# Kernel optimization log

Measured on AMD Instinct MI355X. Metric: run time of the kernel, lower is better.

The kernel has to match this reference:

```python
import jax, jax.numpy as jnp
import numpy as np

N_NODES = 20000
N_EDGES = 160000
IN_DIM = 512
HID = 256
N_CLASSES = 2
NUM_GRAPHS = 16


def setup_inputs() -> dict:
    key = jax.random.key(0)
    ks = jax.random.split(key, 12)
    x = jax.random.normal(ks[0], (N_NODES, IN_DIM), dtype=jnp.float32)
    edge_index = jax.random.randint(ks[1], (2, N_EDGES), 0, N_NODES, dtype=jnp.int64)
    batch = jnp.sort(jax.random.randint(ks[2], (N_NODES,), 0, NUM_GRAPHS, dtype=jnp.int64))
    def glorot(k, shape):
        lim = float(np.sqrt(6.0 / (shape[0] + shape[1])))
        return jax.random.uniform(k, shape, jnp.float32, -lim, lim)
    return {
        "x": x,
        "edge_index": edge_index,
        "batch": batch,
        "W1n": glorot(ks[3], (IN_DIM, HID)),
        "W1s": glorot(ks[4], (IN_DIM, HID)),
        "b1": jnp.zeros((HID,), jnp.float32),
        "W2n": glorot(ks[5], (HID, HID)),
        "W2s": glorot(ks[6], (HID, HID)),
        "b2": jnp.zeros((HID,), jnp.float32),
        "fc1w": glorot(ks[7], (HID, HID // 2)),
        "fc1b": jnp.zeros((HID // 2,), jnp.float32),
        "fc2w": glorot(ks[8], (HID // 2, N_CLASSES)),
        "fc2b": jnp.zeros((N_CLASSES,), jnp.float32),
    }


def _sage_conv(x, W_nbr, W_self, b, src, dst, n_nodes):
    # mean-aggregate neighbor features (messages flow src -> dst, PyG convention)
    deg = jax.ops.segment_sum(jnp.ones(src.shape, x.dtype), dst, num_segments=n_nodes)
    deg = jnp.maximum(deg, 1.0)
    aggr = jax.ops.segment_sum(x[src], dst, num_segments=n_nodes) / deg[:, None]
    # SAGEConv: lin_l(aggr) + lin_r(x) + bias (equivalent to concat-linear)
    return aggr @ W_nbr + x @ W_self + b


def reference(x, edge_index, batch, W1n, W1s, b1, W2n, W2s, b2, fc1w, fc1b, fc2w, fc2b):
    src, dst = edge_index[0], edge_index[1]
    n = x.shape[0]
    h = jax.nn.relu(_sage_conv(x, W1n, W1s, b1, src, dst, n))
    h = jax.nn.relu(_sage_conv(h, W2n, W2s, b2, src, dst, n))
    # global_mean_pool over graph ids
    cnt = jax.ops.segment_sum(jnp.ones((n,), h.dtype), batch, num_segments=NUM_GRAPHS)
    pooled = jax.ops.segment_sum(h, batch, num_segments=NUM_GRAPHS) / jnp.maximum(cnt, 1.0)[:, None]
    out = jax.nn.relu(pooled @ fc1w + fc1b) @ fc2w + fc2b
    return out
```

## Files before the change

### kernel.cpp

```cpp
#include <hip/hip_runtime.h>
#include <hip/hip_bf16.h>


#define HID 256
#define NCOL 512

typedef __bf16 bf16x8 __attribute__((ext_vector_type(8)));
typedef float floatx4 __attribute__((ext_vector_type(4)));
typedef ushort ushort8v __attribute__((ext_vector_type(8)));
typedef unsigned int u32;
typedef const u32 __attribute__((address_space(1)))* gp_t;
typedef u32 __attribute__((address_space(3)))* lp_t;

__device__ __forceinline__ ushort f2bf(float f) {
    unsigned u = __float_as_uint(f);
    u += 0x7fffu + ((u >> 16) & 1u);
    return (ushort)(u >> 16);
}
__device__ __forceinline__ float bf2f(ushort b) {
    return __uint_as_float(((unsigned)b) << 16);
}

__device__ __forceinline__ void packT_work(const float* __restrict__ Wn,
                                           const float* __restrict__ Ws,
                                           ushort* __restrict__ WT, int K, int gid) {
    if (gid >= NCOL * K) return;
    int n = gid / K, k = gid - n * K;
    float v = (n < HID) ? Wn[k * HID + n] : Ws[k * HID + (n - HID)];
    WT[gid] = f2bf(v);
}

__global__ void prep_kernel(const float* __restrict__ x, ushort* __restrict__ xb, int n4,
                            const float* __restrict__ W1n, const float* __restrict__ W1s,
                            ushort* __restrict__ w1t, int K1,
                            const float* __restrict__ W2n, const float* __restrict__ W2s,
                            ushort* __restrict__ w2t, int K2,
                            const int* __restrict__ dst, int* __restrict__ degi, int n_edges,
                            int nb_cvt, int nb_w1, int nb_w2) {
    int bx = blockIdx.x, t = threadIdx.x;
    if (bx < nb_cvt) {
        int i = bx * 256 + t;
        if (i < n4) {
            float4 v = ((const float4*)x)[i];
            ushort4 o;
            o.x = f2bf(v.x); o.y = f2bf(v.y); o.z = f2bf(v.z); o.w = f2bf(v.w);
            ((ushort4*)xb)[i] = o;
        }
    } else if (bx < nb_cvt + nb_w1) {
        packT_work(W1n, W1s, w1t, K1, (bx - nb_cvt) * 256 + t);
    } else if (bx < nb_cvt + nb_w1 + nb_w2) {
        packT_work(W2n, W2s, w2t, K2, (bx - nb_cvt - nb_w1) * 256 + t);
    } else {
        int e = (bx - nb_cvt - nb_w1 - nb_w2) * 256 + t;
        if (e < n_edges) atomicAdd(&degi[dst[e]], 1);
    }
}

__global__ __launch_bounds__(256) void psum_kernel(const int* __restrict__ degi,
                                                   int* __restrict__ partials, int n) {
    int t = threadIdx.x;
    int i = blockIdx.x * 256 + t;
    int v = (i < n) ? degi[i] : 0;
#pragma unroll
    for (int d = 1; d < 64; d <<= 1) v += __shfl_xor(v, d, 64);
    __shared__ int wsum[4];
    if ((t & 63) == 0) wsum[t >> 6] = v;
    __syncthreads();
    if (t == 0) partials[blockIdx.x] = wsum[0] + wsum[1] + wsum[2] + wsum[3];
}

__global__ __launch_bounds__(256) void scan2_kernel(const int* __restrict__ degi,
                                                    const int* __restrict__ partials,
                                                    int* __restrict__ off,
                                                    int* __restrict__ cursor, int n, int nb) {
    int t = threadIdx.x, lane = t & 63, w = t >> 6;
    int c = blockIdx.x;
    int pre = 0, tot = 0;
    for (int base = 0; base < nb; base += 64) {
        int idx = base + lane;
        int pv = (idx < nb) ? partials[idx] : 0;
        pre += (idx < c) ? pv : 0;
        tot += pv;
    }
#pragma unroll
    for (int d = 1; d < 64; d <<= 1) {
        pre += __shfl_xor(pre, d, 64);
        tot += __shfl_xor(tot, d, 64);
    }
    if (c == 0 && t == 0) off[n] = tot;
    int i = c * 256 + t;
    int v = (i < n) ? degi[i] : 0;
    int s = v;
#pragma unroll
    for (int d = 1; d < 64; d <<= 1) {
        int u = __shfl_up(s, d, 64);
        if (lane >= d) s += u;
    }
    __shared__ int wsum[4];
    if (lane == 63) wsum[w] = s;
    __syncthreads();
    int woff = 0;
    for (int k = 0; k < w; ++k) woff += wsum[k];
    int excl = pre + woff + s - v;
    if (i < n) { off[i] = excl; cursor[i] = excl; }
}

__global__ void fill_kernel(const int* __restrict__ src, const int* __restrict__ dst,
                            int* __restrict__ cursor, int* __restrict__ eidx, int n_edges) {
    int e = blockIdx.x * 256 + threadIdx.x;
    if (e < n_edges) {
        int p = atomicAdd(&cursor[dst[e]], 1);
        eidx[p] = src[e];
    }
}

__global__ __launch_bounds__(256) void gemm_mfma(const ushort* __restrict__ A,
                                                 const ushort* __restrict__ BT,
                                                 ushort* __restrict__ Yn,
                                                 ushort* __restrict__ Ys, int K, int nG) {
    int b = blockIdx.x;
    int xcd = b & 7, rest = b >> 3;
    int m = rest & 3, Ggrp = rest >> 2;
    int G = xcd + 8 * Ggrp;
    if (G >= nG) return;
    int m0 = G * 64, n0 = m * 128;

    __shared__ ushort As[2][64 * 64];
    __shared__ ushort Bs[2][128 * 64];
    int tid = threadIdx.x;
    int w = tid >> 6, lane = tid & 63;
    int quad = lane >> 4, r16 = lane & 15;
    int wm = (w >> 1) * 32, wn = (w & 1) * 64;

    int arow[2], agu[2], brow[4], bgu[4];
#pragma unroll
    for (int rr = 0; rr < 2; ++rr) {
        int idx = rr * 256 + tid;
        arow[rr] = idx >> 3;
        agu[rr] = (idx & 7) ^ (arow[rr] & 7);
    }
#pragma unroll
    for (int rr = 0; rr < 4; ++rr) {
        int idx = rr * 256 + tid;
        brow[rr] = idx >> 3;
        bgu[rr] = (idx & 7) ^ (brow[rr] & 7);
    }

    auto stage = [&](int buf, int k0) {
#pragma unroll
        for (int rr = 0; rr < 2; ++rr) {
            const ushort* ga = A + (size_t)(m0 + arow[rr]) * K + k0 + agu[rr] * 8;
            ushort* la = As[buf] + (size_t)(rr * 256 + w * 64) * 8;
            __builtin_amdgcn_global_load_lds((gp_t)(const void*)ga, (lp_t)(void*)la, 16, 0, 0);
        }
#pragma unroll
        for (int rr = 0; rr < 4; ++rr) {
            const ushort* gb = BT + (size_t)(n0 + brow[rr]) * K + k0 + bgu[rr] * 8;
            ushort* lb = Bs[buf] + (size_t)(rr * 256 + w * 64) * 8;
            __builtin_amdgcn_global_load_lds((gp_t)(const void*)gb, (lp_t)(void*)lb, 16, 0, 0);
        }
    };

    floatx4 acc[2][4];
#pragma unroll
    for (int i = 0; i < 2; ++i)
#pragma unroll
        for (int j = 0; j < 4; ++j) acc[i][j] = (floatx4){0.f, 0.f, 0.f, 0.f};

    const int nk = K >> 6;
    stage(0, 0);
    for (int t = 0; t < nk; ++t) {
        int cb = t & 1;
        __syncthreads();
        if (t + 1 < nk) stage(cb ^ 1, (t + 1) << 6);
        const ushort* Ab = As[cb];
        const ushort* Bb = Bs[cb];
#pragma unroll
        for (int s = 0; s < 2; ++s) {
            bf16x8 a[2], b2[4];
#pragma unroll
            for (int i = 0; i < 2; ++i) {
                int row = wm + i * 16 + r16;
                int au = (s * 4 + quad) ^ (row & 7);
                a[i] = *(const bf16x8*)(Ab + row * 64 + au * 8);
            }
#pragma unroll
            for (int j = 0; j < 4; ++j) {
                int row = wn + j * 16 + r16;
                int bu = (s * 4 + quad) ^ (row & 7);
                b2[j] = *(const bf16x8*)(Bb + row * 64 + bu * 8);
            }
#pragma unroll
            for (int i = 0; i < 2; ++i)
#pragma unroll
                for (int j = 0; j < 4; ++j)
                    acc[i][j] = __builtin_amdgcn_mfma_f32_16x16x32_bf16(a[i], b2[j], acc[i][j], 0, 0, 0);
        }
    }
    ushort* O = (m < 2) ? Yn : Ys;
    int cb0 = (m < 2) ? n0 : (n0 - 256);
#pragma unroll
    for (int i = 0; i < 2; ++i)
#pragma unroll
        for (int j = 0; j < 4; ++j) {
            int col = cb0 + wn + j * 16 + r16;
#pragma unroll
            for (int rg = 0; rg < 4; ++rg) {
                int row = m0 + wm + i * 16 + quad * 4 + rg;
                O[(size_t)row * HID + col] = f2bf(acc[i][j][rg]);
            }
        }
}

__device__ __forceinline__ void acc8(float* A, ushort8v y) {
#pragma unroll
    for (int i = 0; i < 8; ++i) A[i] += bf2f((ushort)y[i]);
}

__global__ __launch_bounds__(256) void gather_kernel(const ushort* __restrict__ Yn,
                                                     const ushort* __restrict__ Ys,
                                                     const int* __restrict__ off,
                                                     const int* __restrict__ eidx,
                                                     const float* __restrict__ bias,
                                                     ushort* __restrict__ h, int n_nodes) {
    int tid = threadIdx.x;
    int v = blockIdx.x * 4 + (tid >> 6);
    if (v >= n_nodes) return;
    int lane = tid & 63;
    int half = lane >> 5, sub = lane & 31;
    int c8 = sub << 3;
    int e0 = off[v], e1 = off[v + 1];
    float accA[8] = {0.f, 0.f, 0.f, 0.f, 0.f, 0.f, 0.f, 0.f};
    float accB[8] = {0.f, 0.f, 0.f, 0.f, 0.f, 0.f, 0.f, 0.f};
    for (int base = e0; base < e1; base += 64) {
        int ecnt = min(64, e1 - base);
        int ev = (lane < ecnt) ? eidx[base + lane] : 0;
        int j = 0;
        for (; j + 16 <= ecnt; j += 16) {
            int s0 = __shfl(ev, j + 0 + half, 64);
            int s1 = __shfl(ev, j + 2 + half, 64);
            int s2 = __shfl(ev, j + 4 + half, 64);
            int s3 = __shfl(ev, j + 6 + half, 64);
            int s4 = __shfl(ev, j + 8 + half, 64);
            int s5 = __shfl(ev, j + 10 + half, 64);
            int s6 = __shfl(ev, j + 12 + half, 64);
            int s7 = __shfl(ev, j + 14 + half, 64);
            ushort8v y0 = *(const ushort8v*)(Yn + (size_t)s0 * HID + c8);
            ushort8v y1 = *(const ushort8v*)(Yn + (size_t)s1 * HID + c8);
            ushort8v y2 = *(const ushort8v*)(Yn + (size_t)s2 * HID + c8);
            ushort8v y3 = *(const ushort8v*)(Yn + (size_t)s3 * HID + c8);
            ushort8v y4 = *(const ushort8v*)(Yn + (size_t)s4 * HID + c8);
            ushort8v y5 = *(const ushort8v*)(Yn + (size_t)s5 * HID + c8);
            ushort8v y6 = *(const ushort8v*)(Yn + (size_t)s6 * HID + c8);
            ushort8v y7 = *(const ushort8v*)(Yn + (size_t)s7 * HID + c8);
            acc8(accA, y0); acc8(accB, y1); acc8(accA, y2); acc8(accB, y3);
            acc8(accA, y4); acc8(accB, y5); acc8(accA, y6); acc8(accB, y7);
        }
        for (; j < ecnt; j += 2) {
            int idx = j + half;
            if (idx < ecnt) {
                int s = __shfl(ev, idx, 64);
                ushort8v y = *(const ushort8v*)(Yn + (size_t)s * HID + c8);
                acc8(accA, y);
            }
        }
    }
#pragma unroll
    for (int i = 0; i < 8; ++i) {
        accA[i] += accB[i];
        accA[i] += __shfl_xor(accA[i], 32, 64);
    }
    if (half == 0) {
        ushort8v sv = *(const ushort8v*)(Ys + (size_t)v * HID + c8);
        float bb[8];
        *(float4*)(bb)     = *(const float4*)(bias + c8);
        *(float4*)(bb + 4) = *(const float4*)(bias + c8 + 4);
        float invd = 1.0f / fmaxf((float)(e1 - e0), 1.0f);
        ushort8v r;
#pragma unroll
        for (int i = 0; i < 8; ++i)
            r[i] = f2bf(fmaxf(accA[i] * invd + bf2f((ushort)sv[i]) + bb[i], 0.f));
        *(ushort8v*)(h + (size_t)v * HID + c8) = r;
    }
}

__global__ void pool_kernel(const ushort* __restrict__ h, const int* __restrict__ batch,
                            float* __restrict__ pooled, float* __restrict__ cnt, int n_nodes) {
    int f = threadIdx.x;
    int v0 = blockIdx.x * 64;
    int vend = min(v0 + 64, n_nodes);
    if (v0 >= n_nodes) return;
    int cur = batch[v0];
    float acc = 0.f, ac = 0.f;
    for (int v = v0; v < vend; ++v) {
        int g = batch[v];
        if (g != cur) {
            atomicAdd(&pooled[cur * HID + f], acc);
            if (f == 0) atomicAdd(&cnt[cur], ac);
            acc = 0.f; ac = 0.f; cur = g;
        }
        acc += bf2f(h[(size_t)v * HID + f]);
        ac += 1.0f;
    }
    atomicAdd(&pooled[cur * HID + f], acc);
    if (f == 0) atomicAdd(&cnt[cur], ac);
}

__global__ void head_kernel(const float* __restrict__ pooled, const float* __restrict__ cnt,
                            const float* __restrict__ fc1w, const float* __restrict__ fc1b,
                            const float* __restrict__ fc2w, const float* __restrict__ fc2b,
                            float* __restrict__ out) {
    int g = blockIdx.x, j = threadIdx.x;
    __shared__ float p[256];
    __shared__ float hid[128];
    float inv = 1.0f / fmaxf(cnt[g], 1.0f);
    p[j] = pooled[g * HID + j] * inv;
    p[j + 128] = pooled[g * HID + 128 + j] * inv;
    __syncthreads();
    float a = fc1b[j];
    for (int f = 0; f < 256; ++f) a += p[f] * fc1w[f * 128 + j];
    hid[j] = fmaxf(a, 0.f);
    __syncthreads();
    if (j < 2) {
        float o = fc2b[j];
        for (int t = 0; t < 128; ++t) o += hid[t] * fc2w[t * 2 + j];
        out[g * 2 + j] = o;
    }
}

extern "C" void kernel_launch(void* const* d_in, const int* in_sizes, int n_in,
                              void* d_out, int out_size, void* d_ws, size_t ws_size,
                              hipStream_t stream) {
    const float* x    = (const float*)d_in[0];
    const int*   ei   = (const int*)d_in[1];
    const int*   batch= (const int*)d_in[2];
    const float* W1n  = (const float*)d_in[3];
    const float* W1s  = (const float*)d_in[4];
    const float* b1   = (const float*)d_in[5];
    const float* W2n  = (const float*)d_in[6];
    const float* W2s  = (const float*)d_in[7];
    const float* b2   = (const float*)d_in[8];
    const float* fc1w = (const float*)d_in[9];
    const float* fc1b = (const float*)d_in[10];
    const float* fc2w = (const float*)d_in[11];
    const float* fc2b = (const float*)d_in[12];
    float* out = (float*)d_out;

    const int n_nodes = in_sizes[2];
    const int n_edges = in_sizes[1] / 2;
    const int in_dim  = in_sizes[0] / n_nodes;
    const int Mpad    = (n_nodes + 63) & ~63;
    const int nb      = (n_nodes + 255) / 256;
    const int nG      = Mpad / 64;
    const int* src = ei;
    const int* dst = ei + n_edges;

    char* wsb = (char*)d_ws;
    size_t cur = 0;
    auto alloc = [&](size_t nbytes) { size_t o = cur; cur = (cur + nbytes + 255) & ~(size_t)255; return o; };
    size_t o_degi = alloc((size_t)n_nodes * 4);
    size_t o_pool = alloc((size_t)16 * HID * 4 + 16 * 4);
    size_t zero_end = cur;
    size_t o_off  = alloc((size_t)(n_nodes + 1) * 4);
    size_t o_cur  = alloc((size_t)n_nodes * 4);
    size_t o_part = alloc((size_t)nb * 4);
    size_t o_eidx = alloc((size_t)n_edges * 4);
    size_t o_w1   = alloc((size_t)NCOL * in_dim * 2);
    size_t o_w2   = alloc((size_t)NCOL * HID * 2);
    size_t o_xb   = alloc((size_t)Mpad * in_dim * 2);
    size_t o_hb   = alloc((size_t)Mpad * HID * 2);
    size_t o_yn   = alloc((size_t)Mpad * HID * 2);
    size_t o_ys   = alloc((size_t)Mpad * HID * 2);
    (void)ws_size;

    int*    degi    = (int*)(wsb + o_degi);
    float*  pooled  = (float*)(wsb + o_pool);
    float*  cnt     = pooled + 16 * HID;
    int*    off     = (int*)(wsb + o_off);
    int*    cursor  = (int*)(wsb + o_cur);
    int*    partials= (int*)(wsb + o_part);
    int*    eidx    = (int*)(wsb + o_eidx);
    ushort* w1t     = (ushort*)(wsb + o_w1);
    ushort* w2t     = (ushort*)(wsb + o_w2);
    ushort* xb      = (ushort*)(wsb + o_xb);
    ushort* hb      = (ushort*)(wsb + o_hb);
    ushort* Yn      = (ushort*)(wsb + o_yn);
    ushort* Ys      = (ushort*)(wsb + o_ys);

    hipMemsetAsync(wsb + o_degi, 0, zero_end - o_degi, stream);

    int n4 = n_nodes * in_dim / 4;
    int nb_cvt = (n4 + 255) / 256;
    int nb_w1  = (NCOL * in_dim + 255) / 256;
    int nb_w2  = (NCOL * HID + 255) / 256;
    int nb_deg = (n_edges + 255) / 256;
    prep_kernel<<<nb_cvt + nb_w1 + nb_w2 + nb_deg, 256, 0, stream>>>(
        x, xb, n4, W1n, W1s, w1t, in_dim, W2n, W2s, w2t, HID,
        dst, degi, n_edges, nb_cvt, nb_w1, nb_w2);

    psum_kernel<<<nb, 256, 0, stream>>>(degi, partials, n_nodes);
    scan2_kernel<<<nb, 256, 0, stream>>>(degi, partials, off, cursor, n_nodes, nb);
    fill_kernel<<<(n_edges + 255) / 256, 256, 0, stream>>>(src, dst, cursor, eidx, n_edges);

    int gemm_blocks = 8 * 4 * ((nG + 7) / 8);
    int gather_blocks = (n_nodes + 3) / 4;

    gemm_mfma<<<gemm_blocks, 256, 0, stream>>>(xb, w1t, Yn, Ys, in_dim, nG);
    gather_kernel<<<gather_blocks, 256, 0, stream>>>(Yn, Ys, off, eidx, b1, hb, n_nodes);

    gemm_mfma<<<gemm_blocks, 256, 0, stream>>>(hb, w2t, Yn, Ys, HID, nG);
    gather_kernel<<<gather_blocks, 256, 0, stream>>>(Yn, Ys, off, eidx, b2, hb, n_nodes);

    pool_kernel<<<(n_nodes + 63) / 64, 256, 0, stream>>>(hb, batch, pooled, cnt, n_nodes);
    head_kernel<<<16, 128, 0, stream>>>(pooled, cnt, fc1w, fc1b, fc2w, fc2b, out);
}
```

Measured before the change: 223.7 us.

## Fuse all stages into one persistent kernel with atomic grid barriers

Replaces the sequence of ten kernel launches (prep, scan, fill, two GEMMs, two gathers, pool, head) with a single persistent kernel of 512 blocks that loops over work with grid-stride loops and separates phases with atomic-counter grid barriers. The fill of the CSR edge index now overlaps with the first GEMM in the same phase. This removes per-launch overhead and inter-kernel idle gaps. In exchange, the GEMM and gather lose the XCD-aware tile ordering and the full-grid parallelism, and the barrier spin relies on all 512 blocks being co-resident.

```diff
diff --git a/kernel.cpp b/kernel.cpp
--- a/kernel.cpp
+++ b/kernel.cpp
@@ -4,6 +4,8 @@
 
 #define HID 256
 #define NCOL 512
+#define NB 512
+#define NTHR 256
 
 typedef __bf16 bf16x8 __attribute__((ext_vector_type(8)));
 typedef float floatx4 __attribute__((ext_vector_type(4)));
@@ -21,112 +23,30 @@
     return __uint_as_float(((unsigned)b) << 16);
 }
 
+__device__ __forceinline__ void gsync(u32* bar, int slot) {
+    __syncthreads();
+    if (threadIdx.x == 0) {
+        __threadfence();
+        __hip_atomic_fetch_add(bar + slot, 1u, __ATOMIC_RELEASE, __HIP_MEMORY_SCOPE_AGENT);
+        while (__hip_atomic_load(bar + slot, __ATOMIC_ACQUIRE, __HIP_MEMORY_SCOPE_AGENT) < NB)
+            __builtin_amdgcn_s_sleep(8);
+        __threadfence();
+    }
+    __syncthreads();
+}
+
 __device__ __forceinline__ void packT_work(const float* __restrict__ Wn,
                                            const float* __restrict__ Ws,
                                            ushort* __restrict__ WT, int K, int gid) {
-    if (gid >= NCOL * K) return;
     int n = gid / K, k = gid - n * K;
     float v = (n < HID) ? Wn[k * HID + n] : Ws[k * HID + (n - HID)];
     WT[gid] = f2bf(v);
 }
 
-__global__ void prep_kernel(const float* __restrict__ x, ushort* __restrict__ xb, int n4,
-                            const float* __restrict__ W1n, const float* __restrict__ W1s,
-                            ushort* __restrict__ w1t, int K1,
-                            const float* __restrict__ W2n, const float* __restrict__ W2s,
-                            ushort* __restrict__ w2t, int K2,
-                            const int* __restrict__ dst, int* __restrict__ degi, int n_edges,
-                            int nb_cvt, int nb_w1, int nb_w2) {
-    int bx = blockIdx.x, t = threadIdx.x;
-    if (bx < nb_cvt) {
-        int i = bx * 256 + t;
-        if (i < n4) {
-            float4 v = ((const float4*)x)[i];
-            ushort4 o;
-            o.x = f2bf(v.x); o.y = f2bf(v.y); o.z = f2bf(v.z); o.w = f2bf(v.w);
-            ((ushort4*)xb)[i] = o;
-        }
-    } else if (bx < nb_cvt + nb_w1) {
-        packT_work(W1n, W1s, w1t, K1, (bx - nb_cvt) * 256 + t);
-    } else if (bx < nb_cvt + nb_w1 + nb_w2) {
-        packT_work(W2n, W2s, w2t, K2, (bx - nb_cvt - nb_w1) * 256 + t);
-    } else {
-        int e = (bx - nb_cvt - nb_w1 - nb_w2) * 256 + t;
-        if (e < n_edges) atomicAdd(&degi[dst[e]], 1);
-    }
-}
-
-__global__ __launch_bounds__(256) void psum_kernel(const int* __restrict__ degi,
-                                                   int* __restrict__ partials, int n) {
-    int t = threadIdx.x;
-    int i = blockIdx.x * 256 + t;
-    int v = (i < n) ? degi[i] : 0;
-#pragma unroll
-    for (int d = 1; d < 64; d <<= 1) v += __shfl_xor(v, d, 64);
-    __shared__ int wsum[4];
-    if ((t & 63) == 0) wsum[t >> 6] = v;
-    __syncthreads();
-    if (t == 0) partials[blockIdx.x] = wsum[0] + wsum[1] + wsum[2] + wsum[3];
-}
-
-__global__ __launch_bounds__(256) void scan2_kernel(const int* __restrict__ degi,
-                                                    const int* __restrict__ partials,
-                                                    int* __restrict__ off,
-                                                    int* __restrict__ cursor, int n, int nb) {
-    int t = threadIdx.x, lane = t & 63, w = t >> 6;
-    int c = blockIdx.x;
-    int pre = 0, tot = 0;
-    for (int base = 0; base < nb; base += 64) {
-        int idx = base + lane;
-        int pv = (idx < nb) ? partials[idx] : 0;
-        pre += (idx < c) ? pv : 0;
-        tot += pv;
-    }
-#pragma unroll
-    for (int d = 1; d < 64; d <<= 1) {
-        pre += __shfl_xor(pre, d, 64);
-        tot += __shfl_xor(tot, d, 64);
-    }
-    if (c == 0 && t == 0) off[n] = tot;
-    int i = c * 256 + t;
-    int v = (i < n) ? degi[i] : 0;
-    int s = v;
-#pragma unroll
-    for (int d = 1; d < 64; d <<= 1) {
-        int u = __shfl_up(s, d, 64);
-        if (lane >= d) s += u;
-    }
-    __shared__ int wsum[4];
-    if (lane == 63) wsum[w] = s;
-    __syncthreads();
-    int woff = 0;
-    for (int k = 0; k < w; ++k) woff += wsum[k];
-    int excl = pre + woff + s - v;
-    if (i < n) { off[i] = excl; cursor[i] = excl; }
-}
-
-__global__ void fill_kernel(const int* __restrict__ src, const int* __restrict__ dst,
-                            int* __restrict__ cursor, int* __restrict__ eidx, int n_edges) {
-    int e = blockIdx.x * 256 + threadIdx.x;
-    if (e < n_edges) {
-        int p = atomicAdd(&cursor[dst[e]], 1);
-        eidx[p] = src[e];
-    }
-}
-
-__global__ __launch_bounds__(256) void gemm_mfma(const ushort* __restrict__ A,
-                                                 const ushort* __restrict__ BT,
-                                                 ushort* __restrict__ Yn,
-                                                 ushort* __restrict__ Ys, int K, int nG) {
-    int b = blockIdx.x;
-    int xcd = b & 7, rest = b >> 3;
-    int m = rest & 3, Ggrp = rest >> 2;
-    int G = xcd + 8 * Ggrp;
-    if (G >= nG) return;
-    int m0 = G * 64, n0 = m * 128;
-
-    __shared__ ushort As[2][64 * 64];
-    __shared__ ushort Bs[2][128 * 64];
+__device__ __forceinline__ void gemm_tiles(const ushort* __restrict__ A,
+                                           const ushort* __restrict__ BT,
+                                           ushort* __restrict__ Yn, ushort* __restrict__ Ys,
+                                           int K, int nG, ushort* As0, ushort* Bs0) {
     int tid = threadIdx.x;
     int w = tid >> 6, lane = tid & 63;
     int quad = lane >> 4, r16 = lane & 15;
@@ -146,70 +66,77 @@
         bgu[rr] = (idx & 7) ^ (brow[rr] & 7);
     }
 
-    auto stage = [&](int buf, int k0) {
-#pragma unroll
-        for (int rr = 0; rr < 2; ++rr) {
-            const ushort* ga = A + (size_t)(m0 + arow[rr]) * K + k0 + agu[rr] * 8;
-            ushort* la = As[buf] + (size_t)(rr * 256 + w * 64) * 8;
-            __builtin_amdgcn_global_load_lds((gp_t)(const void*)ga, (lp_t)(void*)la, 16, 0, 0);
-        }
-#pragma unroll
-        for (int rr = 0; rr < 4; ++rr) {
-            const ushort* gb = BT + (size_t)(n0 + brow[rr]) * K + k0 + bgu[rr] * 8;
-            ushort* lb = Bs[buf] + (size_t)(rr * 256 + w * 64) * 8;
-            __builtin_amdgcn_global_load_lds((gp_t)(const void*)gb, (lp_t)(void*)lb, 16, 0, 0);
-        }
-    };
-
-    floatx4 acc[2][4];
-#pragma unroll
-    for (int i = 0; i < 2; ++i)
-#pragma unroll
-        for (int j = 0; j < 4; ++j) acc[i][j] = (floatx4){0.f, 0.f, 0.f, 0.f};
-
-    const int nk = K >> 6;
-    stage(0, 0);
-    for (int t = 0; t < nk; ++t) {
-        int cb = t & 1;
+    const int ntile = nG * 4;
+    for (int tl = blockIdx.x; tl < ntile; tl += NB) {
+        int G = tl >> 2, m = tl & 3;
+        int m0 = G * 64, n0 = m * 128;
+
+        auto stage = [&](int buf, int k0) {
+#pragma unroll
+            for (int rr = 0; rr < 2; ++rr) {
+                const ushort* ga = A + (size_t)(m0 + arow[rr]) * K + k0 + agu[rr] * 8;
+                ushort* la = As0 + (size_t)buf * 4096 + (size_t)(rr * 256 + w * 64) * 8;
+                __builtin_amdgcn_global_load_lds((gp_t)(const void*)ga, (lp_t)(void*)la, 16, 0, 0);
+            }
+#pragma unroll
+            for (int rr = 0; rr < 4; ++rr) {
+                const ushort* gb = BT + (size_t)(n0 + brow[rr]) * K + k0 + bgu[rr] * 8;
+                ushort* lb = Bs0 + (size_t)buf * 8192 + (size_t)(rr * 256 + w * 64) * 8;
+                __builtin_amdgcn_global_load_lds((gp_t)(const void*)gb, (lp_t)(void*)lb, 16, 0, 0);
+            }
+        };
+
+        floatx4 acc[2][4];
+#pragma unroll
+        for (int i = 0; i < 2; ++i)
+#pragma unroll
+            for (int j = 0; j < 4; ++j) acc[i][j] = (floatx4){0.f, 0.f, 0.f, 0.f};
+
         __syncthreads();
-        if (t + 1 < nk) stage(cb ^ 1, (t + 1) << 6);
-        const ushort* Ab = As[cb];
-        const ushort* Bb = Bs[cb];
-#pragma unroll
-        for (int s = 0; s < 2; ++s) {
-            bf16x8 a[2], b2[4];
-#pragma unroll
-            for (int i = 0; i < 2; ++i) {
-                int row = wm + i * 16 + r16;
-                int au = (s * 4 + quad) ^ (row & 7);
-                a[i] = *(const bf16x8*)(Ab + row * 64 + au * 8);
-            }
+        stage(0, 0);
+        const int nk = K >> 6;
+        for (int t = 0; t < nk; ++t) {
+            int cb = t & 1;
+            __syncthreads();
+            if (t + 1 < nk) stage(cb ^ 1, (t + 1) << 6);
+            const ushort* Ab = As0 + cb * 4096;
+            const ushort* Bb = Bs0 + cb * 8192;
+#pragma unroll
+            for (int s = 0; s < 2; ++s) {
+                bf16x8 a[2], b2[4];
+#pragma unroll
+                for (int i = 0; i < 2; ++i) {
+                    int row = wm + i * 16 + r16;
+                    int au = (s * 4 + quad) ^ (row & 7);
+                    a[i] = *(const bf16x8*)(Ab + row * 64 + au * 8);
+                }
+#pragma unroll
+                for (int j = 0; j < 4; ++j) {
+                    int row = wn + j * 16 + r16;
+                    int bu = (s * 4 + quad) ^ (row & 7);
+                    b2[j] = *(const bf16x8*)(Bb + row * 64 + bu * 8);
+                }
+#pragma unroll
+                for (int i = 0; i < 2; ++i)
+#pragma unroll
+                    for (int j = 0; j < 4; ++j)
+                        acc[i][j] = __builtin_amdgcn_mfma_f32_16x16x32_bf16(a[i], b2[j], acc[i][j], 0, 0, 0);
+            }
+        }
+        ushort* O = (m < 2) ? Yn : Ys;
+        int cb0 = (m < 2) ? n0 : (n0 - 256);
+#pragma unroll
+        for (int i = 0; i < 2; ++i)
 #pragma unroll
             for (int j = 0; j < 4; ++j) {
-                int row = wn + j * 16 + r16;
-                int bu = (s * 4 + quad) ^ (row & 7);
-                b2[j] = *(const bf16x8*)(Bb + row * 64 + bu * 8);
-            }
-#pragma unroll
-            for (int i = 0; i < 2; ++i)
-#pragma unroll
-                for (int j = 0; j < 4; ++j)
-                    acc[i][j] = __builtin_amdgcn_mfma_f32_16x16x32_bf16(a[i], b2[j], acc[i][j], 0, 0, 0);
-        }
-    }
-    ushort* O = (m < 2) ? Yn : Ys;
-    int cb0 = (m < 2) ? n0 : (n0 - 256);
-#pragma unroll
-    for (int i = 0; i < 2; ++i)
-#pragma unroll
-        for (int j = 0; j < 4; ++j) {
-            int col = cb0 + wn + j * 16 + r16;
-#pragma unroll
-            for (int rg = 0; rg < 4; ++rg) {
-                int row = m0 + wm + i * 16 + quad * 4 + rg;
-                O[(size_t)row * HID + col] = f2bf(acc[i][j][rg]);
-            }
-        }
+                int col = cb0 + wn + j * 16 + r16;
+#pragma unroll
+                for (int rg = 0; rg < 4; ++rg) {
+                    int row = m0 + wm + i * 16 + quad * 4 + rg;
+                    O[(size_t)row * HID + col] = f2bf(acc[i][j][rg]);
+                }
+            }
+    }
 }
 
 __device__ __forceinline__ void acc8(float* A, ushort8v y) {
@@ -217,114 +144,214 @@
     for (int i = 0; i < 8; ++i) A[i] += bf2f((ushort)y[i]);
 }
 
-__global__ __launch_bounds__(256) void gather_kernel(const ushort* __restrict__ Yn,
-                                                     const ushort* __restrict__ Ys,
-                                                     const int* __restrict__ off,
-                                                     const int* __restrict__ eidx,
-                                                     const float* __restrict__ bias,
-                                                     ushort* __restrict__ h, int n_nodes) {
+__device__ __forceinline__ void gather_nodes(const ushort* __restrict__ Yn,
+                                             const ushort* __restrict__ Ys,
+                                             const int* __restrict__ off,
+                                             const int* __restrict__ eidx,
+                                             const float* __restrict__ bias,
+                                             ushort* __restrict__ h, int n_nodes) {
     int tid = threadIdx.x;
-    int v = blockIdx.x * 4 + (tid >> 6);
-    if (v >= n_nodes) return;
     int lane = tid & 63;
     int half = lane >> 5, sub = lane & 31;
     int c8 = sub << 3;
-    int e0 = off[v], e1 = off[v + 1];
-    float accA[8] = {0.f, 0.f, 0.f, 0.f, 0.f, 0.f, 0.f, 0.f};
-    float accB[8] = {0.f, 0.f, 0.f, 0.f, 0.f, 0.f, 0.f, 0.f};
-    for (int base = e0; base < e1; base += 64) {
-        int ecnt = min(64, e1 - base);
-        int ev = (lane < ecnt) ? eidx[base + lane] : 0;
-        int j = 0;
-        for (; j + 16 <= ecnt; j += 16) {
-            int s0 = __shfl(ev, j + 0 + half, 64);
-            int s1 = __shfl(ev, j + 2 + half, 64);
-            int s2 = __shfl(ev, j + 4 + half, 64);
-            int s3 = __shfl(ev, j + 6 + half, 64);
-            int s4 = __shfl(ev, j + 8 + half, 64);
-            int s5 = __shfl(ev, j + 10 + half, 64);
-            int s6 = __shfl(ev, j + 12 + half, 64);
-            int s7 = __shfl(ev, j + 14 + half, 64);
-            ushort8v y0 = *(const ushort8v*)(Yn + (size_t)s0 * HID + c8);
-            ushort8v y1 = *(const ushort8v*)(Yn + (size_t)s1 * HID + c8);
-            ushort8v y2 = *(const ushort8v*)(Yn + (size_t)s2 * HID + c8);
-            ushort8v y3 = *(const ushort8v*)(Yn + (size_t)s3 * HID + c8);
-            ushort8v y4 = *(const ushort8v*)(Yn + (size_t)s4 * HID + c8);
-            ushort8v y5 = *(const ushort8v*)(Yn + (size_t)s5 * HID + c8);
-            ushort8v y6 = *(const ushort8v*)(Yn + (size_t)s6 * HID + c8);
-            ushort8v y7 = *(const ushort8v*)(Yn + (size_t)s7 * HID + c8);
-            acc8(accA, y0); acc8(accB, y1); acc8(accA, y2); acc8(accB, y3);
-            acc8(accA, y4); acc8(accB, y5); acc8(accA, y6); acc8(accB, y7);
-        }
-        for (; j < ecnt; j += 2) {
-            int idx = j + half;
-            if (idx < ecnt) {
-                int s = __shfl(ev, idx, 64);
-                ushort8v y = *(const ushort8v*)(Yn + (size_t)s * HID + c8);
-                acc8(accA, y);
-            }
-        }
-    }
-#pragma unroll
-    for (int i = 0; i < 8; ++i) {
-        accA[i] += accB[i];
-        accA[i] += __shfl_xor(accA[i], 32, 64);
-    }
-    if (half == 0) {
-        ushort8v sv = *(const ushort8v*)(Ys + (size_t)v * HID + c8);
-        float bb[8];
-        *(float4*)(bb)     = *(const float4*)(bias + c8);
-        *(float4*)(bb + 4) = *(const float4*)(bias + c8 + 4);
-        float invd = 1.0f / fmaxf((float)(e1 - e0), 1.0f);
-        ushort8v r;
-#pragma unroll
-        for (int i = 0; i < 8; ++i)
-            r[i] = f2bf(fmaxf(accA[i] * invd + bf2f((ushort)sv[i]) + bb[i], 0.f));
-        *(ushort8v*)(h + (size_t)v * HID + c8) = r;
-    }
-}
-
-__global__ void pool_kernel(const ushort* __restrict__ h, const int* __restrict__ batch,
-                            float* __restrict__ pooled, float* __restrict__ cnt, int n_nodes) {
-    int f = threadIdx.x;
-    int v0 = blockIdx.x * 64;
-    int vend = min(v0 + 64, n_nodes);
-    if (v0 >= n_nodes) return;
-    int cur = batch[v0];
-    float acc = 0.f, ac = 0.f;
-    for (int v = v0; v < vend; ++v) {
-        int g = batch[v];
-        if (g != cur) {
-            atomicAdd(&pooled[cur * HID + f], acc);
-            if (f == 0) atomicAdd(&cnt[cur], ac);
-            acc = 0.f; ac = 0.f; cur = g;
-        }
-        acc += bf2f(h[(size_t)v * HID + f]);
-        ac += 1.0f;
-    }
-    atomicAdd(&pooled[cur * HID + f], acc);
-    if (f == 0) atomicAdd(&cnt[cur], ac);
-}
-
-__global__ void head_kernel(const float* __restrict__ pooled, const float* __restrict__ cnt,
-                            const float* __restrict__ fc1w, const float* __restrict__ fc1b,
-                            const float* __restrict__ fc2w, const float* __restrict__ fc2b,
-                            float* __restrict__ out) {
-    int g = blockIdx.x, j = threadIdx.x;
-    __shared__ float p[256];
-    __shared__ float hid[128];
-    float inv = 1.0f / fmaxf(cnt[g], 1.0f);
-    p[j] = pooled[g * HID + j] * inv;
-    p[j + 128] = pooled[g * HID + 128 + j] * inv;
-    __syncthreads();
-    float a = fc1b[j];
-    for (int f = 0; f < 256; ++f) a += p[f] * fc1w[f * 128 + j];
-    hid[j] = fmaxf(a, 0.f);
-    __syncthreads();
-    if (j < 2) {
-        float o = fc2b[j];
-        for (int t = 0; t < 128; ++t) o += hid[t] * fc2w[t * 2 + j];
-        out[g * 2 + j] = o;
+    int w0 = (blockIdx.x << 2) + (tid >> 6);
+    for (int v = w0; v < n_nodes; v += NB * 4) {
+        int e0 = off[v], e1 = off[v + 1];
+        float accA[8] = {0.f, 0.f, 0.f, 0.f, 0.f, 0.f, 0.f, 0.f};
+        float accB[8] = {0.f, 0.f, 0.f, 0.f, 0.f, 0.f, 0.f, 0.f};
+        for (int base = e0; base < e1; base += 64) {
+            int ecnt = min(64, e1 - base);
+            int ev = (lane < ecnt) ? eidx[base + lane] : 0;
+            int j = 0;
+            for (; j + 16 <= ecnt; j += 16) {
+                int s0 = __shfl(ev, j + 0 + half, 64);
+                int s1 = __shfl(ev, j + 2 + half, 64);
+                int s2 = __shfl(ev, j + 4 + half, 64);
+                int s3 = __shfl(ev, j + 6 + half, 64);
+                int s4 = __shfl(ev, j + 8 + half, 64);
+                int s5 = __shfl(ev, j + 10 + half, 64);
+                int s6 = __shfl(ev, j + 12 + half, 64);
+                int s7 = __shfl(ev, j + 14 + half, 64);
+                ushort8v y0 = *(const ushort8v*)(Yn + (size_t)s0 * HID + c8);
+                ushort8v y1 = *(const ushort8v*)(Yn + (size_t)s1 * HID + c8);
+                ushort8v y2 = *(const ushort8v*)(Yn + (size_t)s2 * HID + c8);
+                ushort8v y3 = *(const ushort8v*)(Yn + (size_t)s3 * HID + c8);
+                ushort8v y4 = *(const ushort8v*)(Yn + (size_t)s4 * HID + c8);
+                ushort8v y5 = *(const ushort8v*)(Yn + (size_t)s5 * HID + c8);
+                ushort8v y6 = *(const ushort8v*)(Yn + (size_t)s6 * HID + c8);
+                ushort8v y7 = *(const ushort8v*)(Yn + (size_t)s7 * HID + c8);
+                acc8(accA, y0); acc8(accB, y1); acc8(accA, y2); acc8(accB, y3);
+                acc8(accA, y4); acc8(accB, y5); acc8(accA, y6); acc8(accB, y7);
+            }
+            for (; j < ecnt; j += 2) {
+                int idx = j + half;
+                if (idx < ecnt) {
+                    int s = __shfl(ev, idx, 64);
+                    ushort8v y = *(const ushort8v*)(Yn + (size_t)s * HID + c8);
+                    acc8(accA, y);
+                }
+            }
+        }
+#pragma unroll
+        for (int i = 0; i < 8; ++i) {
+            accA[i] += accB[i];
+            accA[i] += __shfl_xor(accA[i], 32, 64);
+        }
+        if (half == 0) {
+            ushort8v sv = *(const ushort8v*)(Ys + (size_t)v * HID + c8);
+            float bb[8];
+            *(float4*)(bb)     = *(const float4*)(bias + c8);
+            *(float4*)(bb + 4) = *(const float4*)(bias + c8 + 4);
+            float invd = 1.0f / fmaxf((float)(e1 - e0), 1.0f);
+            ushort8v r;
+#pragma unroll
+            for (int i = 0; i < 8; ++i)
+                r[i] = f2bf(fmaxf(accA[i] * invd + bf2f((ushort)sv[i]) + bb[i], 0.f));
+            *(ushort8v*)(h + (size_t)v * HID + c8) = r;
+        }
+    }
+}
+
+__global__ __launch_bounds__(NTHR, 2) void mega(
+    const float* __restrict__ x, const int* __restrict__ src, const int* __restrict__ dst,
+    const int* __restrict__ batch,
+    const float* __restrict__ W1n, const float* __restrict__ W1s, const float* __restrict__ b1,
+    const float* __restrict__ W2n, const float* __restrict__ W2s, const float* __restrict__ b2,
+    const float* __restrict__ fc1w, const float* __restrict__ fc1b,
+    const float* __restrict__ fc2w, const float* __restrict__ fc2b,
+    float* __restrict__ out,
+    int* __restrict__ degi, float* __restrict__ pooled, float* __restrict__ cnt,
+    int* __restrict__ off, int* __restrict__ cursor, int* __restrict__ partials,
+    int* __restrict__ eidx, ushort* __restrict__ w1t, ushort* __restrict__ w2t,
+    ushort* __restrict__ xb, ushort* __restrict__ hb,
+    ushort* __restrict__ Yn, ushort* __restrict__ Ys,
+    u32* __restrict__ bar,
+    int n_nodes, int n_edges, int in_dim, int nG, int nbc, int n4) {
+
+    __shared__ ushort As[2 * 64 * 64];
+    __shared__ ushort Bs[2 * 128 * 64];
+    __shared__ int wsum[4];
+
+    const int tid = threadIdx.x, bid = blockIdx.x;
+    const int gthr = bid * NTHR + tid;
+    const int GT = NB * NTHR;
+
+    for (int i = gthr; i < n4; i += GT) {
+        float4 v = ((const float4*)x)[i];
+        ushort4 o;
+        o.x = f2bf(v.x); o.y = f2bf(v.y); o.z = f2bf(v.z); o.w = f2bf(v.w);
+        ((ushort4*)xb)[i] = o;
+    }
+    for (int g = gthr; g < NCOL * in_dim; g += GT) packT_work(W1n, W1s, w1t, in_dim, g);
+    for (int g = gthr; g < NCOL * HID; g += GT) packT_work(W2n, W2s, w2t, HID, g);
+    for (int e = gthr; e < n_edges; e += GT) atomicAdd(&degi[dst[e]], 1);
+    gsync(bar, 0);
+
+    for (int c = bid; c < nbc; c += NB) {
+        int i = c * 256 + tid;
+        int v = (i < n_nodes) ? degi[i] : 0;
+#pragma unroll
+        for (int d = 1; d < 64; d <<= 1) v += __shfl_xor(v, d, 64);
+        if ((tid & 63) == 0) wsum[tid >> 6] = v;
+        __syncthreads();
+        if (tid == 0) partials[c] = wsum[0] + wsum[1] + wsum[2] + wsum[3];
+        __syncthreads();
+    }
+    gsync(bar, 1);
+
+    {
+        int lane = tid & 63, w = tid >> 6;
+        for (int c = bid; c < nbc; c += NB) {
+            int pre = 0, tot = 0;
+            for (int base = 0; base < nbc; base += 64) {
+                int idx = base + lane;
+                int pv = (idx < nbc) ? partials[idx] : 0;
+                pre += (idx < c) ? pv : 0;
+                tot += pv;
+            }
+#pragma unroll
+            for (int d = 1; d < 64; d <<= 1) {
+                pre += __shfl_xor(pre, d, 64);
+                tot += __shfl_xor(tot, d, 64);
+            }
+            if (c == 0 && tid == 0) off[n_nodes] = tot;
+            int i = c * 256 + tid;
+            int v = (i < n_nodes) ? degi[i] : 0;
+            int s = v;
+#pragma unroll
+            for (int d = 1; d < 64; d <<= 1) {
+                int u = __shfl_up(s, d, 64);
+                if (lane >= d) s += u;
+            }
+            if (lane == 63) wsum[w] = s;
+            __syncthreads();
+            int woff = 0;
+            for (int k = 0; k < w; ++k) woff += wsum[k];
+            int excl = pre + woff + s - v;
+            if (i < n_nodes) { off[i] = excl; cursor[i] = excl; }
+            __syncthreads();
+        }
+    }
+    gsync(bar, 2);
+
+    for (int e = gthr; e < n_edges; e += GT) {
+        int p = atomicAdd(&cursor[dst[e]], 1);
+        eidx[p] = src[e];
+    }
+    gemm_tiles(xb, w1t, Yn, Ys, in_dim, nG, As, Bs);
+    gsync(bar, 3);
+
+    gather_nodes(Yn, Ys, off, eidx, b1, hb, n_nodes);
+    gsync(bar, 4);
+
+    gemm_tiles(hb, w2t, Yn, Ys, HID, nG, As, Bs);
+    gsync(bar, 5);
+
+    gather_nodes(Yn, Ys, off, eidx, b2, hb, n_nodes);
+    gsync(bar, 6);
+
+    for (int c = bid; c < (n_nodes + 63) / 64; c += NB) {
+        int v0 = c * 64;
+        int vend = min(v0 + 64, n_nodes);
+        int curg = batch[v0];
+        float acc = 0.f, ac = 0.f;
+        int f = tid;
+        for (int v = v0; v < vend; ++v) {
+            int g = batch[v];
+            if (g != curg) {
+                atomicAdd(&pooled[curg * HID + f], acc);
+                if (f == 0) atomicAdd(&cnt[curg], ac);
+                acc = 0.f; ac = 0.f; curg = g;
+            }
+            acc += bf2f(hb[(size_t)v * HID + f]);
+            ac += 1.0f;
+        }
+        atomicAdd(&pooled[curg * HID + f], acc);
+        if (f == 0) atomicAdd(&cnt[curg], ac);
+    }
+    gsync(bar, 7);
+
+    if (bid < 16) {
+        float* hp = (float*)As;
+        float* hh = hp + 256;
+        int g = bid, j = tid;
+        float inv = 1.0f / fmaxf(cnt[g], 1.0f);
+        if (j < 128) {
+            hp[j] = pooled[g * HID + j] * inv;
+            hp[j + 128] = pooled[g * HID + 128 + j] * inv;
+        }
+        __syncthreads();
+        if (j < 128) {
+            float a = fc1b[j];
+            for (int f = 0; f < 256; ++f) a += hp[f] * fc1w[f * 128 + j];
+            hh[j] = fmaxf(a, 0.f);
+        }
+        __syncthreads();
+        if (j < 2) {
+            float o = fc2b[j];
+            for (int t = 0; t < 128; ++t) o += hh[t] * fc2w[t * 2 + j];
+            out[g * 2 + j] = o;
+        }
     }
 }
 
@@ -350,20 +377,22 @@
     const int n_edges = in_sizes[1] / 2;
     const int in_dim  = in_sizes[0] / n_nodes;
     const int Mpad    = (n_nodes + 63) & ~63;
-    const int nb      = (n_nodes + 255) / 256;
+    const int nbc     = (n_nodes + 255) / 256;
     const int nG      = Mpad / 64;
+    const int n4      = n_nodes * in_dim / 4;
     const int* src = ei;
     const int* dst = ei + n_edges;
 
     char* wsb = (char*)d_ws;
     size_t cur = 0;
     auto alloc = [&](size_t nbytes) { size_t o = cur; cur = (cur + nbytes + 255) & ~(size_t)255; return o; };
+    size_t o_bar  = alloc(64);
     size_t o_degi = alloc((size_t)n_nodes * 4);
     size_t o_pool = alloc((size_t)16 * HID * 4 + 16 * 4);
     size_t zero_end = cur;
     size_t o_off  = alloc((size_t)(n_nodes + 1) * 4);
     size_t o_cur  = alloc((size_t)n_nodes * 4);
-    size_t o_part = alloc((size_t)nb * 4);
+    size_t o_part = alloc((size_t)nbc * 4);
     size_t o_eidx = alloc((size_t)n_edges * 4);
     size_t o_w1   = alloc((size_t)NCOL * in_dim * 2);
     size_t o_w2   = alloc((size_t)NCOL * HID * 2);
@@ -373,6 +402,7 @@
     size_t o_ys   = alloc((size_t)Mpad * HID * 2);
     (void)ws_size;
 
+    u32*    bar     = (u32*)(wsb + o_bar);
     int*    degi    = (int*)(wsb + o_degi);
     float*  pooled  = (float*)(wsb + o_pool);
     float*  cnt     = pooled + 16 * HID;
@@ -387,30 +417,12 @@
     ushort* Yn      = (ushort*)(wsb + o_yn);
     ushort* Ys      = (ushort*)(wsb + o_ys);
 
-    hipMemsetAsync(wsb + o_degi, 0, zero_end - o_degi, stream);
-
-    int n4 = n_nodes * in_dim / 4;
-    int nb_cvt = (n4 + 255) / 256;
-    int nb_w1  = (NCOL * in_dim + 255) / 256;
-    int nb_w2  = (NCOL * HID + 255) / 256;
-    int nb_deg = (n_edges + 255) / 256;
-    prep_kernel<<<nb_cvt + nb_w1 + nb_w2 + nb_deg, 256, 0, stream>>>(
-        x, xb, n4, W1n, W1s, w1t, in_dim, W2n, W2s, w2t, HID,
-        dst, degi, n_edges, nb_cvt, nb_w1, nb_w2);
-
-    psum_kernel<<<nb, 256, 0, stream>>>(degi, partials, n_nodes);
-    scan2_kernel<<<nb, 256, 0, stream>>>(degi, partials, off, cursor, n_nodes, nb);
-    fill_kernel<<<(n_edges + 255) / 256, 256, 0, stream>>>(src, dst, cursor, eidx, n_edges);
-
-    int gemm_blocks = 8 * 4 * ((nG + 7) / 8);
-    int gather_blocks = (n_nodes + 3) / 4;
-
-    gemm_mfma<<<gemm_blocks, 256, 0, stream>>>(xb, w1t, Yn, Ys, in_dim, nG);
-    gather_kernel<<<gather_blocks, 256, 0, stream>>>(Yn, Ys, off, eidx, b1, hb, n_nodes);
-
-    gemm_mfma<<<gemm_blocks, 256, 0, stream>>>(hb, w2t, Yn, Ys, HID, nG);
-    gather_kernel<<<gather_blocks, 256, 0, stream>>>(Yn, Ys, off, eidx, b2, hb, n_nodes);
-
-    pool_kernel<<<(n_nodes + 63) / 64, 256, 0, stream>>>(hb, batch, pooled, cnt, n_nodes);
-    head_kernel<<<16, 128, 0, stream>>>(pooled, cnt, fc1w, fc1b, fc2w, fc2b, out);
-}
+    hipMemsetAsync(wsb + o_bar, 0, zero_end - o_bar, stream);
+
+    mega<<<NB, NTHR, 0, stream>>>(
+        x, src, dst, batch, W1n, W1s, b1, W2n, W2s, b2,
+        fc1w, fc1b, fc2w, fc2b, out,
+        degi, pooled, cnt, off, cursor, partials, eidx,
+        w1t, w2t, xb, hb, Yn, Ys, bar,
+        n_nodes, n_edges, in_dim, nG, nbc, n4);
+}
```

After: 863.6 us. 286% more time.

## Fuse fp32-to-bf16 input conversion into first GEMM and fold edge fill into it

Applied to the files above, without the earlier changes.

The standalone conversion of x to bf16 in the prep kernel is dropped. The first GEMM now reads fp32 rows directly, converts them to bf16 in registers and writes them to LDS, clamping padded rows to the last valid node. The CSR fill kernel is merged into the first GEMM launch as extra trailing blocks, which removes one kernel launch and a full bf16 copy of x written to and read back from memory. In exchange, the first GEMM's A operand loads go through registers instead of direct global-to-LDS copies and read twice as many bytes, which may weaken the load pipelining.

```diff
diff --git a/kernel.cpp b/kernel.cpp
--- a/kernel.cpp
+++ b/kernel.cpp
@@ -30,28 +30,19 @@
     WT[gid] = f2bf(v);
 }
 
-__global__ void prep_kernel(const float* __restrict__ x, ushort* __restrict__ xb, int n4,
-                            const float* __restrict__ W1n, const float* __restrict__ W1s,
+__global__ void prep_kernel(const float* __restrict__ W1n, const float* __restrict__ W1s,
                             ushort* __restrict__ w1t, int K1,
                             const float* __restrict__ W2n, const float* __restrict__ W2s,
                             ushort* __restrict__ w2t, int K2,
                             const int* __restrict__ dst, int* __restrict__ degi, int n_edges,
-                            int nb_cvt, int nb_w1, int nb_w2) {
+                            int nb_w1, int nb_w2) {
     int bx = blockIdx.x, t = threadIdx.x;
-    if (bx < nb_cvt) {
-        int i = bx * 256 + t;
-        if (i < n4) {
-            float4 v = ((const float4*)x)[i];
-            ushort4 o;
-            o.x = f2bf(v.x); o.y = f2bf(v.y); o.z = f2bf(v.z); o.w = f2bf(v.w);
-            ((ushort4*)xb)[i] = o;
-        }
-    } else if (bx < nb_cvt + nb_w1) {
-        packT_work(W1n, W1s, w1t, K1, (bx - nb_cvt) * 256 + t);
-    } else if (bx < nb_cvt + nb_w1 + nb_w2) {
-        packT_work(W2n, W2s, w2t, K2, (bx - nb_cvt - nb_w1) * 256 + t);
+    if (bx < nb_w1) {
+        packT_work(W1n, W1s, w1t, K1, bx * 256 + t);
+    } else if (bx < nb_w1 + nb_w2) {
+        packT_work(W2n, W2s, w2t, K2, (bx - nb_w1) * 256 + t);
     } else {
-        int e = (bx - nb_cvt - nb_w1 - nb_w2) * 256 + t;
+        int e = (bx - nb_w1 - nb_w2) * 256 + t;
         if (e < n_edges) atomicAdd(&degi[dst[e]], 1);
     }
 }
@@ -105,20 +96,26 @@
     if (i < n) { off[i] = excl; cursor[i] = excl; }
 }
 
-__global__ void fill_kernel(const int* __restrict__ src, const int* __restrict__ dst,
-                            int* __restrict__ cursor, int* __restrict__ eidx, int n_edges) {
-    int e = blockIdx.x * 256 + threadIdx.x;
-    if (e < n_edges) {
-        int p = atomicAdd(&cursor[dst[e]], 1);
-        eidx[p] = src[e];
-    }
-}
-
-__global__ __launch_bounds__(256) void gemm_mfma(const ushort* __restrict__ A,
-                                                 const ushort* __restrict__ BT,
-                                                 ushort* __restrict__ Yn,
-                                                 ushort* __restrict__ Ys, int K, int nG) {
+template<int F32A, int DOFILL>
+__global__ __launch_bounds__(256) void gemm_kernel(const void* __restrict__ Av,
+                                                   const ushort* __restrict__ BT,
+                                                   ushort* __restrict__ Yn,
+                                                   ushort* __restrict__ Ys,
+                                                   int K, int nG, int nClamp, int gemmBlocks,
+                                                   const int* __restrict__ src,
+                                                   const int* __restrict__ dst,
+                                                   int* __restrict__ cursor,
+                                                   int* __restrict__ eidx, int n_edges) {
     int b = blockIdx.x;
+    int tid = threadIdx.x;
+    if (DOFILL && b >= gemmBlocks) {
+        int e = (b - gemmBlocks) * 256 + tid;
+        if (e < n_edges) {
+            int p = atomicAdd(&cursor[dst[e]], 1);
+            eidx[p] = src[e];
+        }
+        return;
+    }
     int xcd = b & 7, rest = b >> 3;
     int m = rest & 3, Ggrp = rest >> 2;
     int G = xcd + 8 * Ggrp;
@@ -127,17 +124,21 @@
 
     __shared__ ushort As[2][64 * 64];
     __shared__ ushort Bs[2][128 * 64];
-    int tid = threadIdx.x;
     int w = tid >> 6, lane = tid & 63;
     int quad = lane >> 4, r16 = lane & 15;
     int wm = (w >> 1) * 32, wn = (w & 1) * 64;
 
-    int arow[2], agu[2], brow[4], bgu[4];
+    const ushort* A16 = (const ushort*)Av;
+    const float*  A32 = (const float*)Av;
+
+    int arow[2], agu[2], aridx[2], brow[4], bgu[4];
 #pragma unroll
     for (int rr = 0; rr < 2; ++rr) {
         int idx = rr * 256 + tid;
         arow[rr] = idx >> 3;
         agu[rr] = (idx & 7) ^ (arow[rr] & 7);
+        aridx[rr] = m0 + arow[rr];
+        if (F32A) aridx[rr] = min(aridx[rr], nClamp - 1);
     }
 #pragma unroll
     for (int rr = 0; rr < 4; ++rr) {
@@ -147,11 +148,24 @@
     }
 
     auto stage = [&](int buf, int k0) {
-#pragma unroll
-        for (int rr = 0; rr < 2; ++rr) {
-            const ushort* ga = A + (size_t)(m0 + arow[rr]) * K + k0 + agu[rr] * 8;
-            ushort* la = As[buf] + (size_t)(rr * 256 + w * 64) * 8;
-            __builtin_amdgcn_global_load_lds((gp_t)(const void*)ga, (lp_t)(void*)la, 16, 0, 0);
+        if (F32A) {
+#pragma unroll
+            for (int rr = 0; rr < 2; ++rr) {
+                const float* ga = A32 + (size_t)aridx[rr] * K + k0 + agu[rr] * 8;
+                float4 u0 = *(const float4*)ga;
+                float4 u1 = *(const float4*)(ga + 4);
+                ushort8v o;
+                o[0] = f2bf(u0.x); o[1] = f2bf(u0.y); o[2] = f2bf(u0.z); o[3] = f2bf(u0.w);
+                o[4] = f2bf(u1.x); o[5] = f2bf(u1.y); o[6] = f2bf(u1.z); o[7] = f2bf(u1.w);
+                *(ushort8v*)(As[buf] + (size_t)(rr * 256 + tid) * 8) = o;
+            }
+        } else {
+#pragma unroll
+            for (int rr = 0; rr < 2; ++rr) {
+                const ushort* ga = A16 + (size_t)aridx[rr] * K + k0 + agu[rr] * 8;
+                ushort* la = As[buf] + (size_t)(rr * 256 + w * 64) * 8;
+                __builtin_amdgcn_global_load_lds((gp_t)(const void*)ga, (lp_t)(void*)la, 16, 0, 0);
+            }
         }
 #pragma unroll
         for (int rr = 0; rr < 4; ++rr) {
@@ -367,7 +381,6 @@
     size_t o_eidx = alloc((size_t)n_edges * 4);
     size_t o_w1   = alloc((size_t)NCOL * in_dim * 2);
     size_t o_w2   = alloc((size_t)NCOL * HID * 2);
-    size_t o_xb   = alloc((size_t)Mpad * in_dim * 2);
     size_t o_hb   = alloc((size_t)Mpad * HID * 2);
     size_t o_yn   = alloc((size_t)Mpad * HID * 2);
     size_t o_ys   = alloc((size_t)Mpad * HID * 2);
@@ -382,33 +395,33 @@
     int*    eidx    = (int*)(wsb + o_eidx);
     ushort* w1t     = (ushort*)(wsb + o_w1);
     ushort* w2t     = (ushort*)(wsb + o_w2);
-    ushort* xb      = (ushort*)(wsb + o_xb);
     ushort* hb      = (ushort*)(wsb + o_hb);
     ushort* Yn      = (ushort*)(wsb + o_yn);
     ushort* Ys      = (ushort*)(wsb + o_ys);
 
     hipMemsetAsync(wsb + o_degi, 0, zero_end - o_degi, stream);
 
-    int n4 = n_nodes * in_dim / 4;
-    int nb_cvt = (n4 + 255) / 256;
     int nb_w1  = (NCOL * in_dim + 255) / 256;
     int nb_w2  = (NCOL * HID + 255) / 256;
     int nb_deg = (n_edges + 255) / 256;
-    prep_kernel<<<nb_cvt + nb_w1 + nb_w2 + nb_deg, 256, 0, stream>>>(
-        x, xb, n4, W1n, W1s, w1t, in_dim, W2n, W2s, w2t, HID,
-        dst, degi, n_edges, nb_cvt, nb_w1, nb_w2);
+    prep_kernel<<<nb_w1 + nb_w2 + nb_deg, 256, 0, stream>>>(
+        W1n, W1s, w1t, in_dim, W2n, W2s, w2t, HID, dst, degi, n_edges, nb_w1, nb_w2);
 
     psum_kernel<<<nb, 256, 0, stream>>>(degi, partials, n_nodes);
     scan2_kernel<<<nb, 256, 0, stream>>>(degi, partials, off, cursor, n_nodes, nb);
-    fill_kernel<<<(n_edges + 255) / 256, 256, 0, stream>>>(src, dst, cursor, eidx, n_edges);
 
     int gemm_blocks = 8 * 4 * ((nG + 7) / 8);
+    int fill_blocks = (n_edges + 255) / 256;
     int gather_blocks = (n_nodes + 3) / 4;
 
-    gemm_mfma<<<gemm_blocks, 256, 0, stream>>>(xb, w1t, Yn, Ys, in_dim, nG);
+    gemm_kernel<1, 1><<<gemm_blocks + fill_blocks, 256, 0, stream>>>(
+        x, w1t, Yn, Ys, in_dim, nG, n_nodes, gemm_blocks,
+        src, dst, cursor, eidx, n_edges);
     gather_kernel<<<gather_blocks, 256, 0, stream>>>(Yn, Ys, off, eidx, b1, hb, n_nodes);
 
-    gemm_mfma<<<gemm_blocks, 256, 0, stream>>>(hb, w2t, Yn, Ys, HID, nG);
+    gemm_kernel<0, 0><<<gemm_blocks, 256, 0, stream>>>(
+        hb, w2t, Yn, Ys, HID, nG, 0, gemm_blocks,
+        nullptr, nullptr, nullptr, nullptr, 0);
     gather_kernel<<<gather_blocks, 256, 0, stream>>>(Yn, Ys, off, eidx, b2, hb, n_nodes);
 
     pool_kernel<<<(n_nodes + 63) / 64, 256, 0, stream>>>(hb, batch, pooled, cnt, n_nodes);
```

Result: faster. 217.1 us (-2.9%).
